# Kernel tuning notes

Hardware: AMD Instinct MI355X
Metric: run time of the kernel (lower is better)

Reference implementation:

```python
import jax, jax.numpy as jnp
import numpy as np
import math
from functools import lru_cache

DIM = 64   # num_inputs
HID = 32   # hidden_dim
B = 1024
LOG2 = math.log(2.0)
LOG_2PI = math.log(2.0 * math.pi)


@lru_cache(maxsize=None)
def _masks(out_f, in_f, dim):
    ob, ib = out_f // dim, in_f // dim
    md = np.zeros((out_f, in_f), np.float32)
    mo = np.ones((out_f, in_f), np.float32)
    for i in range(dim):
        md[i * ob:(i + 1) * ob, i * ib:(i + 1) * ib] = 1.0
        mo[i * ob:(i + 1) * ob, i * ib:] = 0.0
    return jnp.asarray(md), jnp.asarray(mo)


def masked_weight(x, grad, W, dw, b, dim):
    # W: (out_f, in_f), dw: (out_f, 1), b: (out_f,)
    out_f, in_f = W.shape
    ob, ib = out_f // dim, in_f // dim
    md, mo = _masks(out_f, in_f, dim)
    w = jnp.exp(W) * md + W * mo                      # positive diag blocks, masked lower blocks
    wsn = jnp.sum(w * w, axis=-1, keepdims=True)      # (out_f, 1) weight-norm denom^2
    wn = jnp.exp(dw) * w / jnp.sqrt(wsn)              # weight-normalized matrix
    wpl = dw + W - 0.5 * jnp.log(wsn)                 # log of diag-block entries, (out_f, in_f)
    # extract diagonal blocks: (dim, ob, dim, ib) -> diag over block index -> (ob, ib, dim)
    blocks = jnp.diagonal(wpl.reshape(dim, ob, dim, ib), axis1=0, axis2=2)
    g = jnp.transpose(blocks, (2, 0, 1))              # (dim, ob, ib) == torch g per-sample
    out = x @ wn.T + b
    if grad is None:
        return out, jnp.broadcast_to(g[None], (x.shape[0],) + g.shape)
    # grad: (Bt, dim, a, c); log-domain block 'matmul' via logsumexp over shared axis a(=ib)
    comb = g[None, :, :, None, :] + jnp.swapaxes(grad, -1, -2)[:, :, None, :, :]  # (Bt,dim,ob,c,ib)
    return out, jax.nn.logsumexp(comb, axis=-1)       # (Bt, dim, ob, c)


def tanh_layer(x, grad):
    g = -2.0 * (x - LOG2 + jax.nn.softplus(-2.0 * x))
    return jnp.tanh(x), g.reshape(grad.shape) + grad


def bnaf_flow(x, p0, p1, p2, gate, dim):
    out, grad = masked_weight(x, None, *p0, dim)
    out, grad = tanh_layer(out, grad)
    out, grad = masked_weight(out, grad, *p1, dim)
    out, grad = tanh_layer(out, grad)
    out, grad = masked_weight(out, grad, *p2, dim)
    g = grad.reshape(grad.shape[0], dim)              # squeeze (B, dim, 1, 1) -> (B, dim)
    if gate is None:
        return out, jnp.sum(g, -1)
    s = jax.nn.sigmoid(gate)
    out = s * out + (1.0 - s) * x
    ldj = jnp.sum(jax.nn.softplus(g + gate) - jax.nn.softplus(gate), -1)
    return out, ldj


def _forward(x, params, gates):
    ldj = 0.0
    for f in range(3):
        gate = gates[f] if f < 2 else None
        x, l = bnaf_flow(x, params[f][0], params[f][1], params[f][2], gate, DIM)
        ldj = ldj + l
        if f < 2:
            x = x[:, ::-1]                            # Permutation('flip'), log-det 0
    log_p_y = jnp.sum(-0.5 * x * x - 0.5 * LOG_2PI, -1)
    return log_p_y + ldj                              # (B,)


def setup_inputs() -> dict:
    key = jax.random.key(0)
    ks = iter(jax.random.split(key, 64))
    d, dh = DIM, DIM * HID
    shapes = [(dh, d), (dh, dh), (d, dh)]
    inp = {"x": jax.random.normal(next(ks), (B, d), jnp.float32)}
    for f in range(3):
        for l, (o, i) in enumerate(shapes):
            inp[f"W{f}_{l}"] = 0.1 * jax.random.normal(next(ks), (o, i), jnp.float32)
            inp[f"dw{f}_{l}"] = jnp.log(jax.random.uniform(next(ks), (o, 1), jnp.float32, 0.1, 1.0))
            inp[f"b{f}_{l}"] = 0.01 * jax.random.normal(next(ks), (o,), jnp.float32)
    inp["gate0"] = jax.random.normal(next(ks), (1,), jnp.float32)
    inp["gate1"] = jax.random.normal(next(ks), (1,), jnp.float32)
    return inp


def reference(x, W0_0, dw0_0, b0_0, W0_1, dw0_1, b0_1, W0_2, dw0_2, b0_2,
              W1_0, dw1_0, b1_0, W1_1, dw1_1, b1_1, W1_2, dw1_2, b1_2,
              W2_0, dw2_0, b2_0, W2_1, dw2_1, b2_1, W2_2, dw2_2, b2_2,
              gate0, gate1):
    params = [
        [(W0_0, dw0_0, b0_0), (W0_1, dw0_1, b0_1), (W0_2, dw0_2, b0_2)],
        [(W1_0, dw1_0, b1_0), (W1_1, dw1_1, b1_1), (W1_2, dw1_2, b1_2)],
        [(W2_0, dw2_0, b2_0), (W2_1, dw2_1, b2_1), (W2_2, dw2_2, b2_2)],
    ]
    return _forward(x, params, (gate0, gate1))
```

## Files before the change

### kernel.cpp

```cpp
#include <hip/hip_runtime.h>
#include <hip/hip_bf16.h>
#include <math.h>


#define DIMN 64
#define BATCH 1024
#define HIDF 2048
#define SPLITK 4
#define NT2 32

typedef __attribute__((ext_vector_type(8))) short short8;
typedef __attribute__((ext_vector_type(4))) float floatx4;
typedef __hip_bfloat16 bf16;

__device__ __forceinline__ float softplusf_(float t) {
    return fmaxf(t, 0.f) + log1pf(__expf(-fabsf(t)));
}

__device__ __forceinline__ float bf2f(short v) {
    union { unsigned u; float f; } x;
    x.u = ((unsigned)(unsigned short)v) << 16;
    return x.f;
}

__device__ __forceinline__ void gl_lds16(const void* g, void* l) {
    __builtin_amdgcn_global_load_lds(
        (const __attribute__((address_space(1))) unsigned int*)g,
        (__attribute__((address_space(3))) unsigned int*)l, 16, 0, 0);
}

__device__ __forceinline__ void tanh_sech2_(float p, float& th, float& s2) {
    float t = __expf(-2.f * fabsf(p));
    float opt = 1.f + t;
    float inv = 1.f / opt;
    th = copysignf((1.f - t) * inv, p);
    s2 = 4.f * t * inv * inv;
}

template<int INF>
__device__ __forceinline__ void prep_row(
    const float* __restrict__ W, const float* __restrict__ dw,
    void* __restrict__ wn_out, float* __restrict__ eg,
    int r, int lane, int out_f, int ob, int ib, int transpose, int bf16out)
{
    constexpr int NI = INF / 64;
    int d = r / ob;
    int c0 = d * ib;
    int c1 = c0 + ib;
    const float* Wr = W + (size_t)r * INF;

    float vv[NI];
    float ss = 0.f;
#pragma unroll
    for (int i = 0; i < NI; ++i) {
        int c = lane + i * 64;
        float wraw = Wr[c];
        float wv = (c < c0) ? wraw : ((c < c1) ? __expf(wraw) : 0.f);
        vv[i] = wv;
        ss += wv * wv;
    }
    for (int off = 32; off > 0; off >>= 1) ss += __shfl_xor(ss, off, 64);

    float dwr = dw[r];
    float scale = __expf(dwr) / sqrtf(ss);
    float logt = dwr - 0.5f * __logf(ss);

#pragma unroll
    for (int i = 0; i < NI; ++i) {
        int c = lane + i * 64;
        float val = scale * vv[i];
        if (bf16out) {
            ((bf16*)wn_out)[(size_t)r * INF + c] = __float2bfloat16(val);
        } else if (transpose) {
            ((float*)wn_out)[(size_t)c * out_f + r] = val;
        } else {
            ((float*)wn_out)[(size_t)r * INF + c] = val;
        }
    }
    if (lane < ib) eg[(size_t)r * ib + lane] = __expf(logt + Wr[c0 + lane]);
}

struct PrepIn { const float *W0, *dw0, *W1, *dw1, *W2, *dw2; };

__global__ __launch_bounds__(64) void prep_mega(
    PrepIn p0, PrepIn p1, PrepIn p2,
    float* __restrict__ wn0T_all, float* __restrict__ eg0_all,
    bf16* __restrict__ wn1_all, float* __restrict__ e1_all,
    bf16* __restrict__ wn2b_all, float* __restrict__ e2_all)
{
    int blk = blockIdx.x;
    int lane = threadIdx.x;
    int f = blk / 4160;
    int rem = blk - f * 4160;
    PrepIn P = (f == 0) ? p0 : ((f == 1) ? p1 : p2);

    float* wn0T = wn0T_all + (size_t)f * DIMN * HIDF;
    float* eg0  = eg0_all  + (size_t)f * HIDF;
    bf16* wn1   = wn1_all + (size_t)f * HIDF * HIDF;
    float* e1   = e1_all   + (size_t)f * HIDF * 32;
    bf16* wn2b  = wn2b_all + (size_t)f * DIMN * HIDF;
    float* e2   = e2_all   + (size_t)f * DIMN * 32;

    if (rem < HIDF) {
        prep_row<DIMN>(P.W0, P.dw0, wn0T, eg0, rem, lane, HIDF, 32, 1, 1, 0);
    } else if (rem < 2 * HIDF) {
        prep_row<HIDF>(P.W1, P.dw1, wn1, e1, rem - HIDF, lane, HIDF, 32, 32, 0, 1);
    } else {
        prep_row<HIDF>(P.W2, P.dw2, wn2b, e2, rem - 2 * HIDF, lane, DIMN, 1, 32, 0, 1);
    }
}

__global__ __launch_bounds__(256) void gemm0_act(
    const float* __restrict__ xin, const float* __restrict__ wn0T,
    const float* __restrict__ bias, const float* __restrict__ eg0,
    bf16* __restrict__ h0, bf16* __restrict__ g0e)
{
    __shared__ float xs[16][DIMN];
    int b0 = blockIdx.y * 16;
    {
        const float4* src = (const float4*)(xin + (size_t)b0 * DIMN);
        ((float4*)xs)[threadIdx.x] = src[threadIdx.x];
    }
    __syncthreads();
    int n = blockIdx.x * 256 + threadIdx.x;

    float acc[16];
#pragma unroll
    for (int j = 0; j < 16; ++j) acc[j] = 0.f;

#pragma unroll 4
    for (int c4 = 0; c4 < 16; ++c4) {
        int c = c4 * 4;
        float w0 = wn0T[(size_t)(c + 0) * HIDF + n];
        float w1 = wn0T[(size_t)(c + 1) * HIDF + n];
        float w2 = wn0T[(size_t)(c + 2) * HIDF + n];
        float w3 = wn0T[(size_t)(c + 3) * HIDF + n];
#pragma unroll
        for (int j = 0; j < 16; ++j) {
            float4 x4 = *(const float4*)&xs[j][c];
            acc[j] = fmaf(x4.x, w0, acc[j]);
            acc[j] = fmaf(x4.y, w1, acc[j]);
            acc[j] = fmaf(x4.z, w2, acc[j]);
            acc[j] = fmaf(x4.w, w3, acc[j]);
        }
    }
    float bv = bias[n], egv = eg0[n];
#pragma unroll
    for (int j = 0; j < 16; ++j) {
        float p = acc[j] + bv;
        float th, s2;
        tanh_sech2_(p, th, s2);
        size_t idx = (size_t)(b0 + j) * HIDF + n;
        h0[idx] = __float2bfloat16(th);
        g0e[idx] = __float2bfloat16(egv * s2);
    }
}

__constant__ unsigned char G1_JN[40] = {
    3,4,5,6,7,7,8,8,9,9,10,10,11,11,11,12,12,12,13,13,13,14,14,14,
    15,15,15,15, 2,6,10,14, 1,5,9,13, 0,4,8,12 };
__constant__ unsigned char G1_KZ[40] = {
    0,0,0,0,0,1,0,1,0,1, 0, 1, 0, 1, 2, 0, 1, 2, 0, 1, 2, 0, 1, 2,
     0, 1, 2, 3, 0,1, 2, 3, 0,1,2,3, 0,1,2,3 };

#define G1BK 64
__global__ __launch_bounds__(256) void gemm1_part(
    const bf16* __restrict__ A, const bf16* __restrict__ B,
    bf16* __restrict__ part)
{
    __shared__ __align__(16) char smem_[65536];
    const int K = HIDF, N = HIDF;
    int pr = blockIdx.x >> 3;
    int my = blockIdx.x & 7;
    int jn = G1_JN[pr];
    int kz = G1_KZ[pr];
    int kbase = kz * (K / SPLITK);
    int kend = (jn + 1) * 128 - kbase;
    if (kend > K / SPLITK) kend = K / SPLITK;

    int tid = threadIdx.x;
    int lane = tid & 63;
    int wave = tid >> 6;
    int n0 = jn * 128;
    int m0 = my * 128;
    int wr = wave >> 1;
    int wc = wave & 1;
    int rf = lane & 15;
    int q = lane >> 4;

    const char* agp[4];
    const char* bgp[4];
    int lofs[4];
#pragma unroll
    for (int s = 0; s < 4; ++s) {
        int c = tid + s * 256;
        int row = c >> 3;
        int kc = (c & 7) ^ (row & 7);
        agp[s] = (const char*)A + ((size_t)(m0 + row) * K + kbase) * 2 + kc * 16;
        bgp[s] = (const char*)B + ((size_t)(n0 + row) * K + kbase) * 2 + kc * 16;
        lofs[s] = c * 16;
    }

    floatx4 acc[4][4];
#pragma unroll
    for (int i = 0; i < 4; ++i)
#pragma unroll
        for (int j = 0; j < 4; ++j) acc[i][j] = (floatx4){0.f, 0.f, 0.f, 0.f};

    int rowA0 = wr * 64 + rf;
    int rowB0 = wc * 64 + rf;

    {
        char* base = smem_;
#pragma unroll
        for (int s = 0; s < 4; ++s) {
            gl_lds16(agp[s], base + lofs[s]);
            gl_lds16(bgp[s], base + 16384 + lofs[s]);
        }
    }
    __syncthreads();

    int cur = 0;
    for (int k0 = 0; k0 < kend; k0 += G1BK) {
        int nk = k0 + G1BK;
        if (nk < kend) {
            size_t kb = (size_t)nk * 2;
            char* base = smem_ + (cur ^ 1) * 32768;
#pragma unroll
            for (int s = 0; s < 4; ++s) {
                gl_lds16(agp[s] + kb, base + lofs[s]);
                gl_lds16(bgp[s] + kb, base + 16384 + lofs[s]);
            }
        }

        const short* As = (const short*)(smem_ + cur * 32768);
        const short* Bs = (const short*)(smem_ + cur * 32768 + 16384);
#pragma unroll
        for (int s = 0; s < 2; ++s) {
            short8 af[4], bfv[4];
#pragma unroll
            for (int i = 0; i < 4; ++i) {
                int row = rowA0 + i * 16;
                af[i] = *(const short8*)&As[row * 64 + (((s * 4 + q) ^ (row & 7)) * 8)];
            }
#pragma unroll
            for (int j = 0; j < 4; ++j) {
                int row = rowB0 + j * 16;
                bfv[j] = *(const short8*)&Bs[row * 64 + (((s * 4 + q) ^ (row & 7)) * 8)];
            }
#pragma unroll
            for (int i = 0; i < 4; ++i)
#pragma unroll
                for (int j = 0; j < 4; ++j)
                    acc[i][j] = __builtin_amdgcn_mfma_f32_16x16x32_bf16(af[i], bfv[j], acc[i][j], 0, 0, 0);
        }
        __syncthreads();
        cur ^= 1;
    }

    bf16* pk = part + (size_t)kz * BATCH * HIDF;
    int col = lane & 15;
    int rq = (lane >> 4) * 4;
#pragma unroll
    for (int i = 0; i < 4; ++i) {
#pragma unroll
        for (int j = 0; j < 4; ++j) {
            int n = n0 + wc * 64 + j * 16 + col;
#pragma unroll
            for (int r = 0; r < 4; ++r) {
                int m = m0 + wr * 64 + i * 16 + rq + r;
                pk[(size_t)m * N + n] = __float2bfloat16(acc[i][j][r]);
            }
        }
    }
}

__global__ __launch_bounds__(256) void act_grad_gemm2(
    const bf16* __restrict__ part, const float* __restrict__ bias,
    const float* __restrict__ e1, const bf16* __restrict__ g0e,
    const bf16* __restrict__ wn2b,
    bf16* __restrict__ grad1e, float* __restrict__ out2p)
{
    __shared__ char smem[17408 + 8704 + 8192];
    float* g0s = (float*)smem;
    short* h1s = (short*)(smem + 17408);
    short* Bs2 = (short*)(smem + 17408 + 8704);

    int tid = threadIdx.x;
    int lane = tid & 63;
    int wave = tid >> 6;
    int bx = blockIdx.x;
    int n0 = bx * 64;
    int b0 = blockIdx.y * 64;
    int np = (bx >> 3) + 1;

    {
        int c0c = tid, c1c = tid + 256;
        int r0 = c0c >> 3, k0c = (c0c & 7) ^ (r0 & 7);
        int r1 = c1c >> 3, k1c = (c1c & 7) ^ (r1 & 7);
        gl_lds16((const char*)wn2b + ((size_t)r0 * HIDF + n0) * 2 + k0c * 16,
                 (char*)Bs2 + c0c * 16);
        gl_lds16((const char*)wn2b + ((size_t)r1 * HIDF + n0) * 2 + k1c * 16,
                 (char*)Bs2 + c1c * 16);
    }

    for (int s = tid; s < 512; s += 256) {
        int row = s >> 3, c8 = s & 7;
        short8 v = *(const short8*)((const short*)g0e +
                                    (size_t)(b0 + row) * HIDF + n0 + c8 * 8);
        float4 lo = { bf2f(v[0]), bf2f(v[1]), bf2f(v[2]), bf2f(v[3]) };
        float4 hi = { bf2f(v[4]), bf2f(v[5]), bf2f(v[6]), bf2f(v[7]) };
        *(float4*)&g0s[row * 68 + c8 * 8] = lo;
        *(float4*)&g0s[row * 68 + c8 * 8 + 4] = hi;
    }

    int g = tid >> 6;
    int nl = tid & 63;
    int n = n0 + nl;

    float4 er[8];
    const float4* e1r = (const float4*)(e1 + (size_t)n * 32);
#pragma unroll
    for (int qq = 0; qq < 8; ++qq) er[qq] = e1r[qq];

    float bv = bias[n];
    int kb2 = nl & 32;
    const bf16* pp0 = part;
    const bf16* pp1 = (np > 1) ? part + (size_t)1 * BATCH * HIDF : part;
    const bf16* pp2 = (np > 2) ? part + (size_t)2 * BATCH * HIDF : part;
    const bf16* pp3 = (np > 3) ? part + (size_t)3 * BATCH * HIDF : part;
    float m1 = (np > 1) ? 1.f : 0.f;
    float m2 = (np > 2) ? 1.f : 0.f;
    float m3 = (np > 3) ? 1.f : 0.f;

    __syncthreads();

#pragma unroll
    for (int t = 0; t < 16; ++t) {
        int bl = g * 16 + t;
        int b = b0 + bl;
        size_t idx = (size_t)b * HIDF + n;
        float l0 = __bfloat162float(pp0[idx]);
        float l1 = __bfloat162float(pp1[idx]);
        float l2 = __bfloat162float(pp2[idx]);
        float l3 = __bfloat162float(pp3[idx]);
        float pre = bv + l0;
        pre = fmaf(m1, l1, pre);
        pre = fmaf(m2, l2, pre);
        pre = fmaf(m3, l3, pre);
        float th, s2;
        tanh_sech2_(pre, th, s2);
        const float* g0row = &g0s[bl * 68 + kb2];
        float dot = 0.f;
#pragma unroll
        for (int qq = 0; qq < 8; ++qq) {
            float4 gv = *(const float4*)&g0row[qq * 4];
            dot = fmaf(gv.x, er[qq].x, dot);
            dot = fmaf(gv.y, er[qq].y, dot);
            dot = fmaf(gv.z, er[qq].z, dot);
            dot = fmaf(gv.w, er[qq].w, dot);
        }
        bf16 thb = __float2bfloat16(th);
        h1s[bl * 68 + nl] = *(const short*)&thb;
        grad1e[idx] = __float2bfloat16(dot * s2);
    }
    __syncthreads();

    int rf = lane & 15;
    int q = lane >> 4;
    floatx4 acc2[4];
#pragma unroll
    for (int j = 0; j < 4; ++j) acc2[j] = (floatx4){0.f, 0.f, 0.f, 0.f};

#pragma unroll
    for (int s = 0; s < 2; ++s) {
        int rowa = wave * 16 + rf;
        short8 af = *(const short8*)&h1s[rowa * 68 + s * 32 + q * 8];
#pragma unroll
        for (int j = 0; j < 4; ++j) {
            int rowb = j * 16 + rf;
            int cp = (s * 4 + q) ^ (rowb & 7);
            short8 bfv = *(const short8*)&Bs2[rowb * 64 + cp * 8];
            acc2[j] = __builtin_amdgcn_mfma_f32_16x16x32_bf16(af, bfv, acc2[j], 0, 0, 0);
        }
    }

    float* outk = out2p + (size_t)bx * BATCH * DIMN;
    int col = lane & 15;
    int rq = (lane >> 4) * 4;
#pragma unroll
    for (int j = 0; j < 4; ++j) {
#pragma unroll
        for (int r = 0; r < 4; ++r) {
            int m = b0 + wave * 16 + rq + r;
            outk[(size_t)m * DIMN + j * 16 + col] = acc2[j][r];
        }
    }
}

__global__ __launch_bounds__(256) void tail_gemm0(
    const float* __restrict__ out2p, const float* __restrict__ b2,
    const float* __restrict__ e2, const bf16* __restrict__ grad1e,
    const float* __restrict__ x_cur, const float* __restrict__ gate,
    float* __restrict__ x_next, float* __restrict__ ldj, int accum_ldj,
    const float* __restrict__ wn0T_n, const float* __restrict__ bias_n,
    const float* __restrict__ eg0_n,
    bf16* __restrict__ h0, bf16* __restrict__ g0e)
{
    __shared__ float xs[4][DIMN];
    int tid = threadIdx.x;
    int row = tid >> 6;
    int b = blockIdx.x * 4 + row;
    int n = tid & 63;

    float o = b2[n];
#pragma unroll
    for (int p = 0; p < NT2; ++p)
        o += out2p[(size_t)p * BATCH * DIMN + (size_t)b * DIMN + n];

    float gt = gate[0];
    float sg = 1.f / (1.f + __expf(-gt));
    float xo = sg * o + (1.f - sg) * x_cur[(size_t)b * DIMN + n];
    x_next[(size_t)b * DIMN + (63 - n)] = xo;
    xs[row][63 - n] = xo;

    const short8* gr = (const short8*)((const short*)grad1e + (size_t)b * HIDF + n * 32);
    const float4* gc = (const float4*)(e2 + n * 32);
    float s = 0.f;
#pragma unroll
    for (int q = 0; q < 4; ++q) {
        short8 a8 = gr[q];
        float4 c0 = gc[2 * q], c1 = gc[2 * q + 1];
        s = fmaf(bf2f(a8[0]), c0.x, s);
        s = fmaf(bf2f(a8[1]), c0.y, s);
        s = fmaf(bf2f(a8[2]), c0.z, s);
        s = fmaf(bf2f(a8[3]), c0.w, s);
        s = fmaf(bf2f(a8[4]), c1.x, s);
        s = fmaf(bf2f(a8[5]), c1.y, s);
        s = fmaf(bf2f(a8[6]), c1.z, s);
        s = fmaf(bf2f(a8[7]), c1.w, s);
    }
    float gF = __logf(fmaxf(s, 1e-45f));
    float contrib = softplusf_(gF + gt) - softplusf_(gt);
    for (int off = 32; off > 0; off >>= 1) contrib += __shfl_xor(contrib, off, 64);
    if (n == 0) ldj[b] = accum_ldj ? (ldj[b] + contrib) : contrib;

    __syncthreads();

    int b0r = blockIdx.x * 4;
#pragma unroll 1
    for (int i = 0; i < 8; ++i) {
        int n2 = tid + (i << 8);
        float a0 = 0.f, a1 = 0.f, a2 = 0.f, a3 = 0.f;
#pragma unroll 8
        for (int c = 0; c < 64; ++c) {
            float w = wn0T_n[(size_t)c * HIDF + n2];
            a0 = fmaf(xs[0][c], w, a0);
            a1 = fmaf(xs[1][c], w, a1);
            a2 = fmaf(xs[2][c], w, a2);
            a3 = fmaf(xs[3][c], w, a3);
        }
        float bv = bias_n[n2], egv = eg0_n[n2];
        float th, s2;
        tanh_sech2_(a0 + bv, th, s2);
        h0[(size_t)(b0r + 0) * HIDF + n2] = __float2bfloat16(th);
        g0e[(size_t)(b0r + 0) * HIDF + n2] = __float2bfloat16(egv * s2);
        tanh_sech2_(a1 + bv, th, s2);
        h0[(size_t)(b0r + 1) * HIDF + n2] = __float2bfloat16(th);
        g0e[(size_t)(b0r + 1) * HIDF + n2] = __float2bfloat16(egv * s2);
        tanh_sech2_(a2 + bv, th, s2);
        h0[(size_t)(b0r + 2) * HIDF + n2] = __float2bfloat16(th);
        g0e[(size_t)(b0r + 2) * HIDF + n2] = __float2bfloat16(egv * s2);
        tanh_sech2_(a3 + bv, th, s2);
        h0[(size_t)(b0r + 3) * HIDF + n2] = __float2bfloat16(th);
        g0e[(size_t)(b0r + 3) * HIDF + n2] = __float2bfloat16(egv * s2);
    }
}

__global__ __launch_bounds__(256) void tail_final(
    const float* __restrict__ out2p, const float* __restrict__ b2,
    const float* __restrict__ e2, const bf16* __restrict__ grad1e,
    const float* __restrict__ ldj, float* __restrict__ out)
{
    int tid = threadIdx.x;
    int b = blockIdx.x * 4 + (tid >> 6);
    int n = tid & 63;

    float o = b2[n];
#pragma unroll
    for (int p = 0; p < NT2; ++p)
        o += out2p[(size_t)p * BATCH * DIMN + (size_t)b * DIMN + n];

    const short8* gr = (const short8*)((const short*)grad1e + (size_t)b * HIDF + n * 32);
    const float4* gc = (const float4*)(e2 + n * 32);
    float s = 0.f;
#pragma unroll
    for (int q = 0; q < 4; ++q) {
        short8 a8 = gr[q];
        float4 c0 = gc[2 * q], c1 = gc[2 * q + 1];
        s = fmaf(bf2f(a8[0]), c0.x, s);
        s = fmaf(bf2f(a8[1]), c0.y, s);
        s = fmaf(bf2f(a8[2]), c0.z, s);
        s = fmaf(bf2f(a8[3]), c0.w, s);
        s = fmaf(bf2f(a8[4]), c1.x, s);
        s = fmaf(bf2f(a8[5]), c1.y, s);
        s = fmaf(bf2f(a8[6]), c1.z, s);
        s = fmaf(bf2f(a8[7]), c1.w, s);
    }
    float gF = __logf(fmaxf(s, 1e-45f));

    float contrib = gF - 0.5f * o * o - 0.91893853320467274f;
    for (int off = 32; off > 0; off >>= 1) contrib += __shfl_xor(contrib, off, 64);
    if (n == 0) out[b] = ldj[b] + contrib;
}

extern "C" void kernel_launch(void* const* d_in, const int* in_sizes, int n_in,
                              void* d_out, int out_size, void* d_ws, size_t ws_size,
                              hipStream_t stream)
{
    (void)in_sizes; (void)n_in; (void)out_size; (void)ws_size;

    const float* x = (const float*)d_in[0];
    const float* gates[2] = { (const float*)d_in[28], (const float*)d_in[29] };

    char* ws = (char*)d_ws;
    size_t ofs = 0;
    auto alloc = [&](size_t bytes) { char* p = ws + ofs; ofs += (bytes + 255) & ~(size_t)255; return p; };

    bf16* wn1_all  = (bf16*)alloc((size_t)3 * HIDF * HIDF * 2);
    bf16* wn2b_all = (bf16*)alloc((size_t)3 * DIMN * HIDF * 2);
    float* wn0T_all = (float*)alloc((size_t)3 * DIMN * HIDF * 4);
    float* eg0_all  = (float*)alloc((size_t)3 * HIDF * 4);
    float* e1_all   = (float*)alloc((size_t)3 * HIDF * 32 * 4);
    float* e2_all   = (float*)alloc((size_t)3 * DIMN * 32 * 4);
    bf16* h0   = (bf16*)alloc((size_t)BATCH * HIDF * 2);
    bf16* part = (bf16*)alloc((size_t)SPLITK * BATCH * HIDF * 2);
    bf16* g0e    = (bf16*)alloc((size_t)BATCH * HIDF * 2);
    bf16* grad1e = (bf16*)alloc((size_t)BATCH * HIDF * 2);
    float* out2p  = (float*)alloc((size_t)NT2 * BATCH * DIMN * 4);
    float* x1     = (float*)alloc((size_t)BATCH * DIMN * 4);
    float* x2     = (float*)alloc((size_t)BATCH * DIMN * 4);
    float* ldj    = (float*)alloc(BATCH * 4);
    float* outp   = (float*)d_out;

    auto W = [&](int f, int i) { return (const float*)d_in[1 + f * 9 + i]; };

    PrepIn p0 = { W(0,0), W(0,1), W(0,3), W(0,4), W(0,6), W(0,7) };
    PrepIn p1 = { W(1,0), W(1,1), W(1,3), W(1,4), W(1,6), W(1,7) };
    PrepIn p2 = { W(2,0), W(2,1), W(2,3), W(2,4), W(2,6), W(2,7) };

    prep_mega<<<dim3(3 * 4160), dim3(64), 0, stream>>>(
        p0, p1, p2, wn0T_all, eg0_all, wn1_all, e1_all, wn2b_all, e2_all);

    gemm0_act<<<dim3(8, BATCH / 16), dim3(256), 0, stream>>>(
        x, wn0T_all, W(0,2), eg0_all, h0, g0e);

    const float* xcur = x;
    float* xnexts[2] = { x1, x2 };

    for (int f = 0; f < 3; ++f) {
        size_t fo1 = (size_t)f * HIDF * HIDF;
        size_t fo2 = (size_t)f * DIMN * HIDF;

        gemm1_part<<<dim3(320), dim3(256), 0, stream>>>(
            h0, wn1_all + fo1, part);

        act_grad_gemm2<<<dim3(HIDF / 64, BATCH / 64), dim3(256), 0, stream>>>(
            part, W(f,5), e1_all + (size_t)f * HIDF * 32, g0e,
            wn2b_all + fo2, grad1e, out2p);

        if (f < 2) {
            tail_gemm0<<<dim3(BATCH / 4), dim3(256), 0, stream>>>(
                out2p, W(f,8), e2_all + (size_t)f * DIMN * 32, grad1e,
                xcur, gates[f], xnexts[f], ldj, f,
                wn0T_all + (size_t)(f + 1) * DIMN * HIDF, W(f + 1, 2),
                eg0_all + (size_t)(f + 1) * HIDF, h0, g0e);
            xcur = xnexts[f];
        } else {
            tail_final<<<dim3(BATCH / 4), dim3(256), 0, stream>>>(
                out2p, W(2,8), e2_all + (size_t)2 * DIMN * 32, grad1e, ldj, outp);
        }
    }
}
```

Baseline: 308.0 us.

## Pack prep rows four per block, single-buffer gemm1, retile tail_gemm0

prep_mega now runs four rows per 256-thread block instead of one row per 64-thread block, which cuts block count and launch overhead. gemm1_part drops its double-buffered LDS pipeline for a single 32KB buffer with sync-load-sync, trading load/compute overlap for lower LDS use and possibly higher occupancy. tail_gemm0 is retiled to a 2D grid of 16 rows by 256 columns with 16 accumulators per thread, reusing each weight load across more batch rows. As a side effect, every x-column block recomputes the out2p reduction for its rows, and only block 0 writes x_next and ldj.

After: 308.1 us. No clear change (+0.0%).

```diff
diff --git a/kernel.cpp b/kernel.cpp
--- a/kernel.cpp
+++ b/kernel.cpp
@@ -82,16 +82,18 @@
 
 struct PrepIn { const float *W0, *dw0, *W1, *dw1, *W2, *dw2; };
 
-__global__ __launch_bounds__(64) void prep_mega(
+__global__ __launch_bounds__(256) void prep_mega(
     PrepIn p0, PrepIn p1, PrepIn p2,
     float* __restrict__ wn0T_all, float* __restrict__ eg0_all,
     bf16* __restrict__ wn1_all, float* __restrict__ e1_all,
     bf16* __restrict__ wn2b_all, float* __restrict__ e2_all)
 {
     int blk = blockIdx.x;
-    int lane = threadIdx.x;
-    int f = blk / 4160;
-    int rem = blk - f * 4160;
+    int wave = threadIdx.x >> 6;
+    int lane = threadIdx.x & 63;
+    int f = blk / 1040;
+    int rem = blk - f * 1040;
+    int rr = rem * 4 + wave;
     PrepIn P = (f == 0) ? p0 : ((f == 1) ? p1 : p2);
 
     float* wn0T = wn0T_all + (size_t)f * DIMN * HIDF;
@@ -101,12 +103,12 @@
     bf16* wn2b  = wn2b_all + (size_t)f * DIMN * HIDF;
     float* e2   = e2_all   + (size_t)f * DIMN * 32;
 
-    if (rem < HIDF) {
-        prep_row<DIMN>(P.W0, P.dw0, wn0T, eg0, rem, lane, HIDF, 32, 1, 1, 0);
-    } else if (rem < 2 * HIDF) {
-        prep_row<HIDF>(P.W1, P.dw1, wn1, e1, rem - HIDF, lane, HIDF, 32, 32, 0, 1);
+    if (rr < HIDF) {
+        prep_row<DIMN>(P.W0, P.dw0, wn0T, eg0, rr, lane, HIDF, 32, 1, 1, 0);
+    } else if (rr < 2 * HIDF) {
+        prep_row<HIDF>(P.W1, P.dw1, wn1, e1, rr - HIDF, lane, HIDF, 32, 32, 0, 1);
     } else {
-        prep_row<HIDF>(P.W2, P.dw2, wn2b, e2, rem - 2 * HIDF, lane, DIMN, 1, 32, 0, 1);
+        prep_row<HIDF>(P.W2, P.dw2, wn2b, e2, rr - 2 * HIDF, lane, DIMN, 1, 32, 0, 1);
     }
 }
 
@@ -168,7 +170,6 @@
     const bf16* __restrict__ A, const bf16* __restrict__ B,
     bf16* __restrict__ part)
 {
-    __shared__ __align__(16) char smem_[65536];
     const int K = HIDF, N = HIDF;
     int pr = blockIdx.x >> 3;
     int my = blockIdx.x & 7;
@@ -178,6 +179,8 @@
     int kend = (jn + 1) * 128 - kbase;
     if (kend > K / SPLITK) kend = K / SPLITK;
 
+    __shared__ short As[128 * 64];
+    __shared__ short Bs[128 * 64];
     int tid = threadIdx.x;
     int lane = tid & 63;
     int wave = tid >> 6;
@@ -190,7 +193,8 @@
 
     const char* agp[4];
     const char* bgp[4];
-    int lofs[4];
+    char* alds[4];
+    char* blds[4];
 #pragma unroll
     for (int s = 0; s < 4; ++s) {
         int c = tid + s * 256;
@@ -198,7 +202,8 @@
         int kc = (c & 7) ^ (row & 7);
         agp[s] = (const char*)A + ((size_t)(m0 + row) * K + kbase) * 2 + kc * 16;
         bgp[s] = (const char*)B + ((size_t)(n0 + row) * K + kbase) * 2 + kc * 16;
-        lofs[s] = c * 16;
+        alds[s] = (char*)As + c * 16;
+        blds[s] = (char*)Bs + c * 16;
     }
 
     floatx4 acc[4][4];
@@ -210,31 +215,16 @@
     int rowA0 = wr * 64 + rf;
     int rowB0 = wc * 64 + rf;
 
-    {
-        char* base = smem_;
+    for (int k0 = 0; k0 < kend; k0 += G1BK) {
+        size_t kb = (size_t)k0 * 2;
+        __syncthreads();
 #pragma unroll
         for (int s = 0; s < 4; ++s) {
-            gl_lds16(agp[s], base + lofs[s]);
-            gl_lds16(bgp[s], base + 16384 + lofs[s]);
-        }
-    }
-    __syncthreads();
-
-    int cur = 0;
-    for (int k0 = 0; k0 < kend; k0 += G1BK) {
-        int nk = k0 + G1BK;
-        if (nk < kend) {
-            size_t kb = (size_t)nk * 2;
-            char* base = smem_ + (cur ^ 1) * 32768;
-#pragma unroll
-            for (int s = 0; s < 4; ++s) {
-                gl_lds16(agp[s] + kb, base + lofs[s]);
-                gl_lds16(bgp[s] + kb, base + 16384 + lofs[s]);
-            }
-        }
-
-        const short* As = (const short*)(smem_ + cur * 32768);
-        const short* Bs = (const short*)(smem_ + cur * 32768 + 16384);
+            gl_lds16(agp[s] + kb, alds[s]);
+            gl_lds16(bgp[s] + kb, blds[s]);
+        }
+        __syncthreads();
+
 #pragma unroll
         for (int s = 0; s < 2; ++s) {
             short8 af[4], bfv[4];
@@ -254,8 +244,6 @@
                 for (int j = 0; j < 4; ++j)
                     acc[i][j] = __builtin_amdgcn_mfma_f32_16x16x32_bf16(af[i], bfv[j], acc[i][j], 0, 0, 0);
         }
-        __syncthreads();
-        cur ^= 1;
     }
 
     bf16* pk = part + (size_t)kz * BATCH * HIDF;
@@ -407,73 +395,87 @@
     const float* __restrict__ eg0_n,
     bf16* __restrict__ h0, bf16* __restrict__ g0e)
 {
-    __shared__ float xs[4][DIMN];
+    __shared__ float xs[16][DIMN];
     int tid = threadIdx.x;
-    int row = tid >> 6;
-    int b = blockIdx.x * 4 + row;
+    int bx = blockIdx.x;
+    int b0 = blockIdx.y * 16;
     int n = tid & 63;
-
-    float o = b2[n];
-#pragma unroll
-    for (int p = 0; p < NT2; ++p)
-        o += out2p[(size_t)p * BATCH * DIMN + (size_t)b * DIMN + n];
+    int rowg = tid >> 6;
 
     float gt = gate[0];
     float sg = 1.f / (1.f + __expf(-gt));
-    float xo = sg * o + (1.f - sg) * x_cur[(size_t)b * DIMN + n];
-    x_next[(size_t)b * DIMN + (63 - n)] = xo;
-    xs[row][63 - n] = xo;
-
-    const short8* gr = (const short8*)((const short*)grad1e + (size_t)b * HIDF + n * 32);
-    const float4* gc = (const float4*)(e2 + n * 32);
-    float s = 0.f;
-#pragma unroll
-    for (int q = 0; q < 4; ++q) {
-        short8 a8 = gr[q];
-        float4 c0 = gc[2 * q], c1 = gc[2 * q + 1];
-        s = fmaf(bf2f(a8[0]), c0.x, s);
-        s = fmaf(bf2f(a8[1]), c0.y, s);
-        s = fmaf(bf2f(a8[2]), c0.z, s);
-        s = fmaf(bf2f(a8[3]), c0.w, s);
-        s = fmaf(bf2f(a8[4]), c1.x, s);
-        s = fmaf(bf2f(a8[5]), c1.y, s);
-        s = fmaf(bf2f(a8[6]), c1.z, s);
-        s = fmaf(bf2f(a8[7]), c1.w, s);
-    }
-    float gF = __logf(fmaxf(s, 1e-45f));
-    float contrib = softplusf_(gF + gt) - softplusf_(gt);
-    for (int off = 32; off > 0; off >>= 1) contrib += __shfl_xor(contrib, off, 64);
-    if (n == 0) ldj[b] = accum_ldj ? (ldj[b] + contrib) : contrib;
-
+    float bv2 = b2[n];
+
+#pragma unroll
+    for (int i = 0; i < 4; ++i) {
+        int row = rowg * 4 + i;
+        int b = b0 + row;
+        float o = bv2;
+#pragma unroll
+        for (int p = 0; p < NT2; ++p)
+            o += out2p[(size_t)p * BATCH * DIMN + (size_t)b * DIMN + n];
+        float xo = sg * o + (1.f - sg) * x_cur[(size_t)b * DIMN + n];
+        xs[row][63 - n] = xo;
+
+        if (bx == 0) {
+            x_next[(size_t)b * DIMN + (63 - n)] = xo;
+            const short8* gr = (const short8*)((const short*)grad1e +
+                                               (size_t)b * HIDF + n * 32);
+            const float4* gc = (const float4*)(e2 + n * 32);
+            float s = 0.f;
+#pragma unroll
+            for (int q = 0; q < 4; ++q) {
+                short8 a8 = gr[q];
+                float4 c0 = gc[2 * q], c1 = gc[2 * q + 1];
+                s = fmaf(bf2f(a8[0]), c0.x, s);
+                s = fmaf(bf2f(a8[1]), c0.y, s);
+                s = fmaf(bf2f(a8[2]), c0.z, s);
+                s = fmaf(bf2f(a8[3]), c0.w, s);
+                s = fmaf(bf2f(a8[4]), c1.x, s);
+                s = fmaf(bf2f(a8[5]), c1.y, s);
+                s = fmaf(bf2f(a8[6]), c1.z, s);
+                s = fmaf(bf2f(a8[7]), c1.w, s);
+            }
+            float gF = __logf(fmaxf(s, 1e-45f));
+            float contrib = softplusf_(gF + gt) - softplusf_(gt);
+            for (int off = 32; off > 0; off >>= 1)
+                contrib += __shfl_xor(contrib, off, 64);
+            if (n == 0) ldj[b] = accum_ldj ? (ldj[b] + contrib) : contrib;
+        }
+    }
     __syncthreads();
 
-    int b0r = blockIdx.x * 4;
-#pragma unroll 1
-    for (int i = 0; i < 8; ++i) {
-        int n2 = tid + (i << 8);
-        float a0 = 0.f, a1 = 0.f, a2 = 0.f, a3 = 0.f;
-#pragma unroll 8
-        for (int c = 0; c < 64; ++c) {
-            float w = wn0T_n[(size_t)c * HIDF + n2];
-            a0 = fmaf(xs[0][c], w, a0);
-            a1 = fmaf(xs[1][c], w, a1);
-            a2 = fmaf(xs[2][c], w, a2);
-            a3 = fmaf(xs[3][c], w, a3);
-        }
-        float bv = bias_n[n2], egv = eg0_n[n2];
+    int nn = bx * 256 + tid;
+
+    float acc[16];
+#pragma unroll
+    for (int j = 0; j < 16; ++j) acc[j] = 0.f;
+
+#pragma unroll 4
+    for (int c4 = 0; c4 < 16; ++c4) {
+        int c = c4 * 4;
+        float w0 = wn0T_n[(size_t)(c + 0) * HIDF + nn];
+        float w1 = wn0T_n[(size_t)(c + 1) * HIDF + nn];
+        float w2 = wn0T_n[(size_t)(c + 2) * HIDF + nn];
+        float w3 = wn0T_n[(size_t)(c + 3) * HIDF + nn];
+#pragma unroll
+        for (int j = 0; j < 16; ++j) {
+            float4 x4 = *(const float4*)&xs[j][c];
+            acc[j] = fmaf(x4.x, w0, acc[j]);
+            acc[j] = fmaf(x4.y, w1, acc[j]);
+            acc[j] = fmaf(x4.z, w2, acc[j]);
+            acc[j] = fmaf(x4.w, w3, acc[j]);
+        }
+    }
+    float bvn = bias_n[nn], egv = eg0_n[nn];
+#pragma unroll
+    for (int j = 0; j < 16; ++j) {
+        float p = acc[j] + bvn;
         float th, s2;
-        tanh_sech2_(a0 + bv, th, s2);
-        h0[(size_t)(b0r + 0) * HIDF + n2] = __float2bfloat16(th);
-        g0e[(size_t)(b0r + 0) * HIDF + n2] = __float2bfloat16(egv * s2);
-        tanh_sech2_(a1 + bv, th, s2);
-        h0[(size_t)(b0r + 1) * HIDF + n2] = __float2bfloat16(th);
-        g0e[(size_t)(b0r + 1) * HIDF + n2] = __float2bfloat16(egv * s2);
-        tanh_sech2_(a2 + bv, th, s2);
-        h0[(size_t)(b0r + 2) * HIDF + n2] = __float2bfloat16(th);
-        g0e[(size_t)(b0r + 2) * HIDF + n2] = __float2bfloat16(egv * s2);
-        tanh_sech2_(a3 + bv, th, s2);
-        h0[(size_t)(b0r + 3) * HIDF + n2] = __float2bfloat16(th);
-        g0e[(size_t)(b0r + 3) * HIDF + n2] = __float2bfloat16(egv * s2);
+        tanh_sech2_(p, th, s2);
+        size_t idx = (size_t)(b0 + j) * HIDF + nn;
+        h0[idx] = __float2bfloat16(th);
+        g0e[idx] = __float2bfloat16(egv * s2);
     }
 }
 
@@ -549,7 +551,7 @@
     PrepIn p1 = { W(1,0), W(1,1), W(1,3), W(1,4), W(1,6), W(1,7) };
     PrepIn p2 = { W(2,0), W(2,1), W(2,3), W(2,4), W(2,6), W(2,7) };
 
-    prep_mega<<<dim3(3 * 4160), dim3(64), 0, stream>>>(
+    prep_mega<<<dim3(3 * 1040), dim3(256), 0, stream>>>(
         p0, p1, p2, wn0T_all, eg0_all, wn1_all, e1_all, wn2b_all, e2_all);
 
     gemm0_act<<<dim3(8, BATCH / 16), dim3(256), 0, stream>>>(
@@ -570,7 +572,7 @@
             wn2b_all + fo2, grad1e, out2p);
 
         if (f < 2) {
-            tail_gemm0<<<dim3(BATCH / 4), dim3(256), 0, stream>>>(
+            tail_gemm0<<<dim3(8, BATCH / 16), dim3(256), 0, stream>>>(
                 out2p, W(f,8), e2_all + (size_t)f * DIMN * 32, grad1e,
                 xcur, gates[f], xnexts[f], ldj, f,
                 wn0T_all + (size_t)(f + 1) * DIMN * HIDF, W(f + 1, 2),
```
